# Kernel tuning notes

Measured on AMD Instinct MI355X. Metric: run time of the kernel, lower is better.

Reference implementation:

```python
import jax, jax.numpy as jnp
import numpy as np

K = 3            # kernel_size
ZETA = 1e-3      # crf_zeta
NUM_ITER = 2     # crf_num_iter
TOL = 0.0        # tolerance


def unfold3(x):
    """torch.nn.Unfold(3, stride=1, padding=1): [B,C,H,W] -> [B,C,9,H*W].
    Channel-major, kernel positions row-major (matches torch ordering)."""
    B, C, H, W = x.shape
    xp = jnp.pad(x, ((0, 0), (0, 0), (1, 1), (1, 1)))
    patches = jnp.stack(
        [xp[:, :, i:i + H, j:j + W] for i in range(K) for j in range(K)], axis=2
    )  # [B,C,9,H,W]
    return patches.reshape(B, C, K * K, H * W)


def setup_inputs() -> dict:
    key = jax.random.key(0)
    k1, k2, k3 = jax.random.split(key, 3)
    B, C, H, W, D = 2, 3, 256, 704, 64
    # scale color to O(zeta) so the gaussian affinity kernel is non-degenerate
    color = jax.random.normal(k1, (B, C, H, W), dtype=jnp.float32) * ZETA
    feats = jax.random.normal(k2, (B, C, H, W), dtype=jnp.float32)  # unused by forward, kept for signature fidelity
    logits = jax.random.normal(k3, (B, D, H, W), dtype=jnp.float32)
    ws = jnp.full((1,), 0.015, dtype=jnp.float32)  # learned weight self.ws[0]
    return {"color": color, "feats": feats, "logits": logits, "ws": ws}


def reference(color, feats, logits, ws):
    B, C, H, W = color.shape
    D = logits.shape[1]
    HW = H * W

    # gaussian affinity kernel from guide image: [B, 9, HW]
    uc = unfold3(color)  # [B,C,9,HW]
    kernel = jnp.exp(-(((uc - color.reshape(B, C, 1, HW)) ** 2)
                       / (2.0 * ZETA ** 2)).sum(1))

    # label compatibility matrix miu: [D, D]
    idx = jnp.arange(D)
    miu = jnp.clip(jnp.abs(idx[:, None] - idx[None, :]).astype(jnp.float32) - TOL, 0.0)

    logits_flat = logits.reshape(B, D, HW)
    q = jax.nn.softmax(logits, axis=1)
    for _ in range(NUM_ITER):
        uq = unfold3(q)  # [B,D,9,HW]
        q_tilde = (uq * kernel[:, None]).sum(2) * ws  # [B,D,HW]
        q_hat = jnp.einsum('de,ben->bdn', miu, q_tilde)  # [B,D,HW]
        q = jax.nn.softmax(logits_flat - q_hat, axis=1).reshape(B, D, H, W)
    return q
```

## Files before the change

### kernel.cpp

```cpp
#include <hip/hip_runtime.h>
#include <hip/hip_fp16.h>

#define HH 256
#define WW 704
#define DD 64
#define CC 3
#define BB 2
#define HWN (HH * WW)

#define TY 8
#define TX 16
#define RY0 12
#define RX0 20
#define NP0 (RY0 * RX0)
#define RY1 10
#define RX1 18
#define NP1 (RY1 * RX1)
#define NTX (WW / TX)
#define NTY (HH / TY)
#define NTILES (NTX * NTY)

static constexpr float INV2Z2 = 1.0f / (2.0f * 1e-3f * 1e-3f);

__global__ __launch_bounds__(256) void affinity_kernel(
    const float* __restrict__ color, const float* __restrict__ wsp,
    float* __restrict__ kaff)
{
    int n = blockIdx.x * 256 + threadIdx.x;
    int b = blockIdx.y;
    int h = n / WW, w = n - h * WW;
    float wsv = wsp[0];

    const float* cb = color + (size_t)b * CC * HWN + n;
    float c0 = cb[0], c1 = cb[HWN], c2 = cb[2 * HWN];
    bool hm = h > 0, hp = h < HH - 1, wm = w > 0, wp = w < WW - 1;

    float* kb = kaff + (size_t)b * 9 * HWN + n;
#pragma unroll
    for (int dh = -1; dh <= 1; ++dh) {
#pragma unroll
        for (int dw = -1; dw <= 1; ++dw) {
            int k = (dh + 1) * 3 + (dw + 1);
            bool valid = (dh < 0 ? hm : (dh > 0 ? hp : true)) &&
                         (dw < 0 ? wm : (dw > 0 ? wp : true));
            int off = valid ? (dh * WW + dw) : 0;
            float u0 = valid ? cb[off] : 0.f;
            float u1 = valid ? cb[HWN + off] : 0.f;
            float u2 = valid ? cb[2 * HWN + off] : 0.f;
            float d0 = u0 - c0, d1 = u1 - c1, d2 = u2 - c2;
            float ss = d0 * d0 + d1 * d1 + d2 * d2;
            kb[(size_t)k * HWN] = wsv * __expf(-ss * INV2Z2);
        }
    }
}

__device__ __forceinline__ void acc_tap(const unsigned* q, int p0, int cg,
                                        __half2 kh, __half2* tv2) {
    int ia = p0 * 32 + ((cg * 8) ^ ((p0 & 7) << 2));
    int ib = ia ^ 4;
    const __half2* qa = (const __half2*)&q[ia];
    const __half2* qb = (const __half2*)&q[ib];
    tv2[0] = __hfma2(kh, qa[0], tv2[0]);
    tv2[1] = __hfma2(kh, qa[1], tv2[1]);
    tv2[2] = __hfma2(kh, qa[2], tv2[2]);
    tv2[3] = __hfma2(kh, qa[3], tv2[3]);
    tv2[4] = __hfma2(kh, qb[0], tv2[4]);
    tv2[5] = __hfma2(kh, qb[1], tv2[5]);
    tv2[6] = __hfma2(kh, qb[2], tv2[6]);
    tv2[7] = __hfma2(kh, qb[3], tv2[7]);
}

__device__ __forceinline__ void st_px(unsigned* q, int p, int cg,
                                      const float* u, float scale) {
    int ia = p * 32 + ((cg * 8) ^ ((p & 7) << 2));
    int ib = ia ^ 4;
    __half2* qa = (__half2*)&q[ia];
    __half2* qb = (__half2*)&q[ib];
    qa[0] = __floats2half2_rn(u[0]  * scale, u[1]  * scale);
    qa[1] = __floats2half2_rn(u[2]  * scale, u[3]  * scale);
    qa[2] = __floats2half2_rn(u[4]  * scale, u[5]  * scale);
    qa[3] = __floats2half2_rn(u[6]  * scale, u[7]  * scale);
    qb[0] = __floats2half2_rn(u[8]  * scale, u[9]  * scale);
    qb[1] = __floats2half2_rn(u[10] * scale, u[11] * scale);
    qb[2] = __floats2half2_rn(u[12] * scale, u[13] * scale);
    qb[3] = __floats2half2_rn(u[14] * scale, u[15] * scale);
}

__device__ __forceinline__ void scan4(float Aloc, float Bloc, int pxl, int cg,
                                      float& Ar, float& Br, float& T, float& E) {
    float A0 = __shfl(Aloc, pxl),      A1 = __shfl(Aloc, pxl + 16),
          A2 = __shfl(Aloc, pxl + 32), A3 = __shfl(Aloc, pxl + 48);
    float B0 = __shfl(Bloc, pxl),      B1 = __shfl(Bloc, pxl + 16),
          B2 = __shfl(Bloc, pxl + 32), B3 = __shfl(Bloc, pxl + 48);
    T = A0 + A1 + A2 + A3;  E = B0 + B1 + B2 + B3;
    Ar = 0.f; Br = 0.f;
    if (cg > 0) { Ar += A0; Br += B0; }
    if (cg > 1) { Ar += A1; Br += B1; }
    if (cg > 2) { Ar += A2; Br += B2; }
}

__device__ __forceinline__ float finish_px(float* tv, const float* lg,
                                           int pxl, int cg) {
    float Aloc = 0.f, Bloc = 0.f;
#pragma unroll
    for (int i = 0; i < 16; ++i) {
        float e = (float)(cg * 16 + i);
        Aloc += tv[i]; Bloc += e * tv[i];
    }
    float Ar, Br, T, E;
    scan4(Aloc, Bloc, pxl, cg, Ar, Br, T, E);
    float s = 0.f;
#pragma unroll
    for (int i = 0; i < 16; ++i) {
        float e = (float)(cg * 16 + i);
        Ar += tv[i]; Br += e * tv[i];
        float v = lg[(size_t)i * HWN] - (2.f * (e * Ar - Br) + E - e * T);
        tv[i] = __expf(v); s += tv[i];
    }
    s += __shfl_xor(s, 16);
    s += __shfl_xor(s, 32);
    return 1.f / s;
}

__device__ __forceinline__ void load_k(const float* kfb, int n, int gy, int gx,
                                       float* k) {
#pragma unroll
    for (int j = 0; j < 9; ++j) k[j] = kfb[(size_t)j * HWN + n];
    if (gy <= 0)      { k[0] = k[1] = k[2] = 0.f; }
    if (gy >= HH - 1) { k[6] = k[7] = k[8] = 0.f; }
    if (gx <= 0)      { k[0] = k[3] = k[6] = 0.f; }
    if (gx >= WW - 1) { k[2] = k[5] = k[8] = 0.f; }
}

__device__ __forceinline__ void stencil9(const unsigned* qs, int rowstride,
                                         int py, int px, int cg,
                                         const float* k, float* tv) {
    __half2 tv2[8];
#pragma unroll
    for (int j = 0; j < 8; ++j) tv2[j] = __float2half2_rn(0.f);
    int base = (py + 1) * rowstride + (px + 1);
#pragma unroll
    for (int tap = 0; tap < 9; ++tap) {
        int dy = tap / 3 - 1, dx = tap - (tap / 3) * 3 - 1;
        acc_tap(qs, base + dy * rowstride + dx, cg, __float2half2_rn(k[tap]), tv2);
    }
#pragma unroll
    for (int j = 0; j < 8; ++j) {
        float2 f = __half22float2(tv2[j]);
        tv[2 * j] = f.x; tv[2 * j + 1] = f.y;
    }
}

__global__ __launch_bounds__(256) void fused_crf_kernel(
    const float* __restrict__ logits, const float* __restrict__ kaff,
    float* __restrict__ qout)
{
    __shared__ unsigned q0s[NP0 * 32];
    __shared__ unsigned q1s[NP1 * 32];

    const int t = threadIdx.x;
    const int lane = t & 63;
    const int wv = t >> 6;
    const int pxl = lane & 15;
    const int cg = lane >> 4;
    const int b = blockIdx.y;

    const int bid = blockIdx.x;
    const int pb = (bid & 7) * (NTILES / 8) + (bid >> 3);
    const int tyr = pb / NTX, txc = pb - tyr * NTX;
    const int y0 = tyr * TY, x0 = txc * TX;

    const float* lgb = logits + ((size_t)b * DD + cg * 16) * HWN;
    const float* kfb = kaff + (size_t)b * 9 * HWN;

    for (int r = 0; r < 4; ++r) {
        int id = r * 64 + wv * 16 + pxl;
        if (id < NP0) {
            int py = id / RX0, px = id - py * RX0;
            int gy = min(max(y0 - 2 + py, 0), HH - 1);
            int gx = min(max(x0 - 2 + px, 0), WW - 1);
            const float* lg = lgb + gy * WW + gx;
            float v[16];
            float s = 0.f;
#pragma unroll
            for (int i = 0; i < 16; ++i) {
                v[i] = __expf(lg[(size_t)i * HWN]);
                s += v[i];
            }
            s += __shfl_xor(s, 16);
            s += __shfl_xor(s, 32);
            st_px(q0s, id, cg, v, 1.0f / s);
        }
    }
    __syncthreads();

    for (int r = 0; r < 3; ++r) {
        int id = r * 64 + wv * 16 + pxl;
        if (id < NP1) {
            int py = id / RX1, px = id - py * RX1;
            int gy = y0 - 1 + py, gx = x0 - 1 + px;
            int cy = min(max(gy, 0), HH - 1), cx = min(max(gx, 0), WW - 1);
            int n = cy * WW + cx;

            float k[9];
            load_k(kfb, n, gy, gx, k);

            float tv[16];
            stencil9(q0s, RX0, py, px, cg, k, tv);
            float inv = finish_px(tv, lgb + n, pxl, cg);
            st_px(q1s, id, cg, tv, inv);
        }
    }
    __syncthreads();

    for (int r = 0; r < 2; ++r) {
        int id = r * 64 + wv * 16 + pxl;
        int py = id / TX, px = id - py * TX;
        int gy = y0 + py, gx = x0 + px;
        int n = gy * WW + gx;

        float k[9];
        load_k(kfb, n, gy, gx, k);

        float tv[16];
        stencil9(q1s, RX1, py, px, cg, k, tv);
        float inv = finish_px(tv, lgb + n, pxl, cg);

        float* qo = qout + ((size_t)b * DD + cg * 16) * HWN + n;
#pragma unroll
        for (int i = 0; i < 16; ++i) qo[(size_t)i * HWN] = tv[i] * inv;
    }
}

extern "C" void kernel_launch(void* const* d_in, const int* in_sizes, int n_in,
                              void* d_out, int out_size, void* d_ws, size_t ws_size,
                              hipStream_t stream) {
    const float* color  = (const float*)d_in[0];
    const float* logits = (const float*)d_in[2];
    const float* wsp    = (const float*)d_in[3];

    float* q_out = (float*)d_out;
    float* kaff  = (float*)d_ws;

    dim3 gridA(HWN / 256, BB);
    affinity_kernel<<<gridA, 256, 0, stream>>>(color, wsp, kaff);

    dim3 gridF(NTILES, BB);
    fused_crf_kernel<<<gridF, 256, 0, stream>>>(logits, kaff, q_out);
}
```

Measured before the change: 98.62 us.

## Vectorize affinity kernel to four pixels per thread and coalesce halo pixel mapping

```diff
diff --git a/kernel.cpp b/kernel.cpp
--- a/kernel.cpp
+++ b/kernel.cpp
@@ -26,31 +26,66 @@
     const float* __restrict__ color, const float* __restrict__ wsp,
     float* __restrict__ kaff)
 {
-    int n = blockIdx.x * 256 + threadIdx.x;
+    int q = blockIdx.x * 256 + threadIdx.x;
     int b = blockIdx.y;
-    int h = n / WW, w = n - h * WW;
+    int n0 = q * 4;
+    int h = n0 / WW, w0 = n0 - h * WW;
     float wsv = wsp[0];
 
-    const float* cb = color + (size_t)b * CC * HWN + n;
-    float c0 = cb[0], c1 = cb[HWN], c2 = cb[2 * HWN];
-    bool hm = h > 0, hp = h < HH - 1, wm = w > 0, wp = w < WW - 1;
-
-    float* kb = kaff + (size_t)b * 9 * HWN + n;
-#pragma unroll
-    for (int dh = -1; dh <= 1; ++dh) {
-#pragma unroll
-        for (int dw = -1; dw <= 1; ++dw) {
-            int k = (dh + 1) * 3 + (dw + 1);
-            bool valid = (dh < 0 ? hm : (dh > 0 ? hp : true)) &&
-                         (dw < 0 ? wm : (dw > 0 ? wp : true));
-            int off = valid ? (dh * WW + dw) : 0;
-            float u0 = valid ? cb[off] : 0.f;
-            float u1 = valid ? cb[HWN + off] : 0.f;
-            float u2 = valid ? cb[2 * HWN + off] : 0.f;
-            float d0 = u0 - c0, d1 = u1 - c1, d2 = u2 - c2;
-            float ss = d0 * d0 + d1 * d1 + d2 * d2;
-            kb[(size_t)k * HWN] = wsv * __expf(-ss * INV2Z2);
-        }
+    bool hm = h > 0, hp = h < HH - 1;
+    bool wm = w0 > 0, wp = w0 + 4 < WW;
+    int oN = hm ? -WW : 0, oS = hp ? WW : 0;
+    int dl = wm ? -1 : 0, dr = wp ? 4 : 3;
+    float rowm = hm ? 1.f : 0.f, rowp = hp ? 1.f : 0.f;
+    float colm = wm ? 1.f : 0.f, colp = wp ? 1.f : 0.f;
+
+    const float* cbase = color + (size_t)b * CC * HWN + n0;
+
+    float ss[9][4];
+#pragma unroll
+    for (int t9 = 0; t9 < 9; ++t9)
+#pragma unroll
+        for (int j = 0; j < 4; ++j) ss[t9][j] = 0.f;
+
+#pragma unroll
+    for (int ch = 0; ch < 3; ++ch) {
+        const float* cc = cbase + (size_t)ch * HWN;
+        float4 C0 = *(const float4*)cc;
+        float4 Cn = *(const float4*)(cc + oN);
+        float4 Cs = *(const float4*)(cc + oS);
+        float lN = cc[oN + dl], rN = cc[oN + dr];
+        float l0 = cc[dl],      r0 = cc[dr];
+        float lS = cc[oS + dl], rS = cc[oS + dr];
+        Cn.x *= rowm; Cn.y *= rowm; Cn.z *= rowm; Cn.w *= rowm;
+        Cs.x *= rowp; Cs.y *= rowp; Cs.z *= rowp; Cs.w *= rowp;
+        lN *= rowm * colm; rN *= rowm * colp;
+        l0 *= colm;        r0 *= colp;
+        lS *= rowp * colm; rS *= rowp * colp;
+
+        float wN[6]  = {lN, Cn.x, Cn.y, Cn.z, Cn.w, rN};
+        float wC[6]  = {l0, C0.x, C0.y, C0.z, C0.w, r0};
+        float wS[6]  = {lS, Cs.x, Cs.y, Cs.z, Cs.w, rS};
+        float c4[4]  = {C0.x, C0.y, C0.z, C0.w};
+#pragma unroll
+        for (int dw = 0; dw < 3; ++dw)
+#pragma unroll
+            for (int j = 0; j < 4; ++j) {
+                float d;
+                d = wN[j + dw] - c4[j]; ss[0 + dw][j] += d * d;
+                d = wC[j + dw] - c4[j]; ss[3 + dw][j] += d * d;
+                d = wS[j + dw] - c4[j]; ss[6 + dw][j] += d * d;
+            }
+    }
+
+    float* kb = kaff + (size_t)b * 9 * HWN + n0;
+#pragma unroll
+    for (int t9 = 0; t9 < 9; ++t9) {
+        float4 o;
+        o.x = wsv * __expf(-ss[t9][0] * INV2Z2);
+        o.y = wsv * __expf(-ss[t9][1] * INV2Z2);
+        o.z = wsv * __expf(-ss[t9][2] * INV2Z2);
+        o.w = wsv * __expf(-ss[t9][3] * INV2Z2);
+        *(float4*)(kb + (size_t)t9 * HWN) = o;
     }
 }
 
@@ -99,7 +134,7 @@
     if (cg > 2) { Ar += A2; Br += B2; }
 }
 
-__device__ __forceinline__ float finish_px(float* tv, const float* lg,
+__device__ __forceinline__ float finish_px(float* tv, const float* lgv,
                                            int pxl, int cg) {
     float Aloc = 0.f, Bloc = 0.f;
 #pragma unroll
@@ -114,7 +149,7 @@
     for (int i = 0; i < 16; ++i) {
         float e = (float)(cg * 16 + i);
         Ar += tv[i]; Br += e * tv[i];
-        float v = lg[(size_t)i * HWN] - (2.f * (e * Ar - Br) + E - e * T);
+        float v = lgv[i] - (2.f * (e * Ar - Br) + E - e * T);
         tv[i] = __expf(v); s += tv[i];
     }
     s += __shfl_xor(s, 16);
@@ -176,7 +211,10 @@
     for (int r = 0; r < 4; ++r) {
         int id = r * 64 + wv * 16 + pxl;
         if (id < NP0) {
-            int py = id / RX0, px = id - py * RX0;
+            int py, px;
+            if (id < 192) { py = id >> 4; px = id & 15; }
+            else { int qq = id - 192; py = qq >> 2; px = 16 + (qq & 3); }
+            int p = py * RX0 + px;
             int gy = min(max(y0 - 2 + py, 0), HH - 1);
             int gx = min(max(x0 - 2 + px, 0), WW - 1);
             const float* lg = lgb + gy * WW + gx;
@@ -189,7 +227,7 @@
             }
             s += __shfl_xor(s, 16);
             s += __shfl_xor(s, 32);
-            st_px(q0s, id, cg, v, 1.0f / s);
+            st_px(q0s, p, cg, v, 1.0f / s);
         }
     }
     __syncthreads();
@@ -197,34 +235,45 @@
     for (int r = 0; r < 3; ++r) {
         int id = r * 64 + wv * 16 + pxl;
         if (id < NP1) {
-            int py = id / RX1, px = id - py * RX1;
+            int py, px;
+            if (id < 160) { py = id >> 4; px = id & 15; }
+            else { int qq = id - 160; py = qq >> 1; px = 16 + (qq & 1); }
+            int p = py * RX1 + px;
             int gy = y0 - 1 + py, gx = x0 - 1 + px;
             int cy = min(max(gy, 0), HH - 1), cx = min(max(gx, 0), WW - 1);
             int n = cy * WW + cx;
 
             float k[9];
             load_k(kfb, n, gy, gx, k);
+            const float* lgn = lgb + n;
+            float lgv[16];
+#pragma unroll
+            for (int i = 0; i < 16; ++i) lgv[i] = lgn[(size_t)i * HWN];
 
             float tv[16];
             stencil9(q0s, RX0, py, px, cg, k, tv);
-            float inv = finish_px(tv, lgb + n, pxl, cg);
-            st_px(q1s, id, cg, tv, inv);
+            float inv = finish_px(tv, lgv, pxl, cg);
+            st_px(q1s, p, cg, tv, inv);
         }
     }
     __syncthreads();
 
     for (int r = 0; r < 2; ++r) {
         int id = r * 64 + wv * 16 + pxl;
-        int py = id / TX, px = id - py * TX;
+        int py = id >> 4, px = id & 15;
         int gy = y0 + py, gx = x0 + px;
         int n = gy * WW + gx;
 
         float k[9];
         load_k(kfb, n, gy, gx, k);
+        const float* lgn = lgb + n;
+        float lgv[16];
+#pragma unroll
+        for (int i = 0; i < 16; ++i) lgv[i] = lgn[(size_t)i * HWN];
 
         float tv[16];
         stencil9(q1s, RX1, py, px, cg, k, tv);
-        float inv = finish_px(tv, lgb + n, pxl, cg);
+        float inv = finish_px(tv, lgv, pxl, cg);
 
         float* qo = qout + ((size_t)b * DD + cg * 16) * HWN + n;
 #pragma unroll
@@ -242,7 +291,7 @@
     float* q_out = (float*)d_out;
     float* kaff  = (float*)d_ws;
 
-    dim3 gridA(HWN / 256, BB);
+    dim3 gridA(HWN / 4 / 256, BB);
     affinity_kernel<<<gridA, 256, 0, stream>>>(color, wsp, kaff);
 
     dim3 gridF(NTILES, BB);
```

New measurement: 105.5 us. 7.0% more time.

## Precompute initial softmax to global fp16 buffer and read stencil taps from global

Applied to the files above, without the earlier changes.

```diff
diff --git a/kernel.cpp b/kernel.cpp
--- a/kernel.cpp
+++ b/kernel.cpp
@@ -10,9 +10,6 @@
 
 #define TY 8
 #define TX 16
-#define RY0 12
-#define RX0 20
-#define NP0 (RY0 * RX0)
 #define RY1 10
 #define RX1 18
 #define NP1 (RY1 * RX1)
@@ -52,6 +49,37 @@
             kb[(size_t)k * HWN] = wsv * __expf(-ss * INV2Z2);
         }
     }
+}
+
+__global__ __launch_bounds__(256) void q0softmax_kernel(
+    const float* __restrict__ logits, unsigned* __restrict__ q0g)
+{
+    const int t = threadIdx.x, lane = t & 63, wv = t >> 6;
+    const int pxl = lane & 15, cg = lane >> 4;
+    const int n = blockIdx.x * 64 + wv * 16 + pxl;
+    const int b = blockIdx.y;
+
+    const float* lg = logits + ((size_t)b * DD + cg * 16) * HWN + n;
+    float v[16];
+    float s = 0.f;
+#pragma unroll
+    for (int i = 0; i < 16; ++i) {
+        v[i] = __expf(lg[(size_t)i * HWN]);
+        s += v[i];
+    }
+    s += __shfl_xor(s, 16);
+    s += __shfl_xor(s, 32);
+    float inv = 1.0f / s;
+
+    __half2* qp = (__half2*)(q0g + ((size_t)b * HWN + n) * 32 + cg * 8);
+    qp[0] = __floats2half2_rn(v[0]  * inv, v[1]  * inv);
+    qp[1] = __floats2half2_rn(v[2]  * inv, v[3]  * inv);
+    qp[2] = __floats2half2_rn(v[4]  * inv, v[5]  * inv);
+    qp[3] = __floats2half2_rn(v[6]  * inv, v[7]  * inv);
+    qp[4] = __floats2half2_rn(v[8]  * inv, v[9]  * inv);
+    qp[5] = __floats2half2_rn(v[10] * inv, v[11] * inv);
+    qp[6] = __floats2half2_rn(v[12] * inv, v[13] * inv);
+    qp[7] = __floats2half2_rn(v[14] * inv, v[15] * inv);
 }
 
 __device__ __forceinline__ void acc_tap(const unsigned* q, int p0, int cg,
@@ -70,6 +98,20 @@
     tv2[7] = __hfma2(kh, qb[3], tv2[7]);
 }
 
+__device__ __forceinline__ void acc_tap_g(const unsigned* qp, __half2 kh,
+                                          __half2* tv2) {
+    const __half2* qa = (const __half2*)qp;
+    const __half2* qb = (const __half2*)(qp + 4);
+    tv2[0] = __hfma2(kh, qa[0], tv2[0]);
+    tv2[1] = __hfma2(kh, qa[1], tv2[1]);
+    tv2[2] = __hfma2(kh, qa[2], tv2[2]);
+    tv2[3] = __hfma2(kh, qa[3], tv2[3]);
+    tv2[4] = __hfma2(kh, qb[0], tv2[4]);
+    tv2[5] = __hfma2(kh, qb[1], tv2[5]);
+    tv2[6] = __hfma2(kh, qb[2], tv2[6]);
+    tv2[7] = __hfma2(kh, qb[3], tv2[7]);
+}
+
 __device__ __forceinline__ void st_px(unsigned* q, int p, int cg,
                                       const float* u, float scale) {
     int ia = p * 32 + ((cg * 8) ^ ((p & 7) << 2));
@@ -99,7 +141,7 @@
     if (cg > 2) { Ar += A2; Br += B2; }
 }
 
-__device__ __forceinline__ float finish_px(float* tv, const float* lg,
+__device__ __forceinline__ float finish_px(float* tv, const float* lgv,
                                            int pxl, int cg) {
     float Aloc = 0.f, Bloc = 0.f;
 #pragma unroll
@@ -114,7 +156,7 @@
     for (int i = 0; i < 16; ++i) {
         float e = (float)(cg * 16 + i);
         Ar += tv[i]; Br += e * tv[i];
-        float v = lg[(size_t)i * HWN] - (2.f * (e * Ar - Br) + E - e * T);
+        float v = lgv[i] - (2.f * (e * Ar - Br) + E - e * T);
         tv[i] = __expf(v); s += tv[i];
     }
     s += __shfl_xor(s, 16);
@@ -153,9 +195,8 @@
 
 __global__ __launch_bounds__(256) void fused_crf_kernel(
     const float* __restrict__ logits, const float* __restrict__ kaff,
-    float* __restrict__ qout)
+    const unsigned* __restrict__ q0g, float* __restrict__ qout)
 {
-    __shared__ unsigned q0s[NP0 * 32];
     __shared__ unsigned q1s[NP1 * 32];
 
     const int t = threadIdx.x;
@@ -172,27 +213,7 @@
 
     const float* lgb = logits + ((size_t)b * DD + cg * 16) * HWN;
     const float* kfb = kaff + (size_t)b * 9 * HWN;
-
-    for (int r = 0; r < 4; ++r) {
-        int id = r * 64 + wv * 16 + pxl;
-        if (id < NP0) {
-            int py = id / RX0, px = id - py * RX0;
-            int gy = min(max(y0 - 2 + py, 0), HH - 1);
-            int gx = min(max(x0 - 2 + px, 0), WW - 1);
-            const float* lg = lgb + gy * WW + gx;
-            float v[16];
-            float s = 0.f;
-#pragma unroll
-            for (int i = 0; i < 16; ++i) {
-                v[i] = __expf(lg[(size_t)i * HWN]);
-                s += v[i];
-            }
-            s += __shfl_xor(s, 16);
-            s += __shfl_xor(s, 32);
-            st_px(q0s, id, cg, v, 1.0f / s);
-        }
-    }
-    __syncthreads();
+    const unsigned* q0b = q0g + (size_t)b * HWN * 32;
 
     for (int r = 0; r < 3; ++r) {
         int id = r * 64 + wv * 16 + pxl;
@@ -204,10 +225,39 @@
 
             float k[9];
             load_k(kfb, n, gy, gx, k);
+            const float* lgn = lgb + n;
+            float lgv[16];
+#pragma unroll
+            for (int i = 0; i < 16; ++i) lgv[i] = lgn[(size_t)i * HWN];
+
+            int rU = min(max(gy - 1, 0), HH - 1);
+            int rD = min(max(gy + 1, 0), HH - 1);
+            int dl = (cx > 0) ? -32 : 0;
+            int dr = (cx < WW - 1) ? 32 : 0;
+            const unsigned* pU = q0b + ((size_t)rU * WW + cx) * 32 + cg * 8;
+            const unsigned* pM = q0b + ((size_t)cy * WW + cx) * 32 + cg * 8;
+            const unsigned* pD = q0b + ((size_t)rD * WW + cx) * 32 + cg * 8;
+
+            __half2 tv2[8];
+#pragma unroll
+            for (int j = 0; j < 8; ++j) tv2[j] = __float2half2_rn(0.f);
+            acc_tap_g(pU + dl, __float2half2_rn(k[0]), tv2);
+            acc_tap_g(pU,      __float2half2_rn(k[1]), tv2);
+            acc_tap_g(pU + dr, __float2half2_rn(k[2]), tv2);
+            acc_tap_g(pM + dl, __float2half2_rn(k[3]), tv2);
+            acc_tap_g(pM,      __float2half2_rn(k[4]), tv2);
+            acc_tap_g(pM + dr, __float2half2_rn(k[5]), tv2);
+            acc_tap_g(pD + dl, __float2half2_rn(k[6]), tv2);
+            acc_tap_g(pD,      __float2half2_rn(k[7]), tv2);
+            acc_tap_g(pD + dr, __float2half2_rn(k[8]), tv2);
 
             float tv[16];
-            stencil9(q0s, RX0, py, px, cg, k, tv);
-            float inv = finish_px(tv, lgb + n, pxl, cg);
+#pragma unroll
+            for (int j = 0; j < 8; ++j) {
+                float2 f = __half22float2(tv2[j]);
+                tv[2 * j] = f.x; tv[2 * j + 1] = f.y;
+            }
+            float inv = finish_px(tv, lgv, pxl, cg);
             st_px(q1s, id, cg, tv, inv);
         }
     }
@@ -215,16 +265,20 @@
 
     for (int r = 0; r < 2; ++r) {
         int id = r * 64 + wv * 16 + pxl;
-        int py = id / TX, px = id - py * TX;
+        int py = id >> 4, px = id & 15;
         int gy = y0 + py, gx = x0 + px;
         int n = gy * WW + gx;
 
         float k[9];
         load_k(kfb, n, gy, gx, k);
+        const float* lgn = lgb + n;
+        float lgv[16];
+#pragma unroll
+        for (int i = 0; i < 16; ++i) lgv[i] = lgn[(size_t)i * HWN];
 
         float tv[16];
         stencil9(q1s, RX1, py, px, cg, k, tv);
-        float inv = finish_px(tv, lgb + n, pxl, cg);
+        float inv = finish_px(tv, lgv, pxl, cg);
 
         float* qo = qout + ((size_t)b * DD + cg * 16) * HWN + n;
 #pragma unroll
@@ -241,10 +295,14 @@
 
     float* q_out = (float*)d_out;
     float* kaff  = (float*)d_ws;
+    unsigned* q0g = (unsigned*)((float*)d_ws + (size_t)BB * 9 * HWN);
 
     dim3 gridA(HWN / 256, BB);
     affinity_kernel<<<gridA, 256, 0, stream>>>(color, wsp, kaff);
 
+    dim3 gridQ(HWN / 64, BB);
+    q0softmax_kernel<<<gridQ, 256, 0, stream>>>(logits, q0g);
+
     dim3 gridF(NTILES, BB);
-    fused_crf_kernel<<<gridF, 256, 0, stream>>>(logits, kaff, q_out);
-}
+    fused_crf_kernel<<<gridF, 256, 0, stream>>>(logits, kaff, q0g, q_out);
+}
```

Measured after the change: 135.4 us. +37.2%, slower.
